# Optimization experiments

Measured on AMD Instinct MI355X. Metric: run time of the kernel, lower is better.

The kernel has to match this reference:

```python
import jax, jax.numpy as jnp
import numpy as np

S, D, H, DH = 4096, 768, 12, 64
POST_SCALE = float(np.sqrt(384.0))  # division by sqrt(1/384)


def setup_inputs() -> dict:
    key = jax.random.key(0)
    ks = jax.random.split(key, 9)
    std = 1.0 / np.sqrt(D)
    mk = lambda k: (jax.random.uniform(k, (D, D), jnp.float32, -std, std))
    return {
        "x": jax.random.normal(ks[0], (S, D), jnp.float32),
        "Wq": mk(ks[1]), "bq": jax.random.uniform(ks[2], (D,), jnp.float32, -std, std),
        "Wk": mk(ks[3]), "bk": jax.random.uniform(ks[4], (D,), jnp.float32, -std, std),
        "Wv": mk(ks[5]), "bv": jax.random.uniform(ks[6], (D,), jnp.float32, -std, std),
        "Wo": mk(ks[7]), "bo": jax.random.uniform(ks[8], (D,), jnp.float32, -std, std),
    }


def reference(x, Wq, bq, Wk, bk, Wv, bv, Wo, bo):
    # Linear layers (torch convention: y = x @ W.T + b)
    q = (x @ Wq.T + bq).reshape(S, H, DH).transpose(1, 2, 0)  # [H, DH, S]
    k = (x @ Wk.T + bk).reshape(S, H, DH).transpose(1, 0, 2)  # [H, S, DH]
    v = (x @ Wv.T + bv).reshape(S, H, DH).transpose(1, 0, 2)  # [H, S, DH]
    scores = jnp.einsum('hsd,hdt->hst', k, q)                 # [H, S, S] = k @ q
    # nn.Softmax() on a 3-D tensor legacy-defaults to dim=0 (head axis);
    # then post-softmax scale by 1/sqrt(1/384) = sqrt(384)
    attn = jax.nn.softmax(scores, axis=0) * POST_SCALE
    out = jnp.einsum('hst,htd->hsd', attn, v)                 # [H, S, DH]
    out = out.transpose(1, 0, 2).reshape(S, D)                # [S, 768]
    return out @ Wo.T + bo
```

## Files before the change

kernel.cpp:

```cpp
#include <hip/hip_runtime.h>

#define DEVINL __device__ __forceinline__

typedef __attribute__((ext_vector_type(8))) short bf16x8;
typedef __attribute__((ext_vector_type(4))) float f32x4;

static constexpr int S = 4096;
static constexpr int D = 768;
static constexpr float POST_SCALE = 19.595917942265423f;

#define MFMA16(a, b, c) __builtin_amdgcn_mfma_f32_16x16x32_bf16((a), (b), (c), 0, 0, 0)

DEVINL unsigned short f2bf(float f) {
  union { float f; unsigned u; } v; v.f = f;
  unsigned r = (v.u + 0x7FFFu + ((v.u >> 16) & 1u)) >> 16;
  return (unsigned short)r;
}

__global__ void cvt_kernel(const float* __restrict__ src,
                           unsigned short* __restrict__ dst, int n4) {
  int i = blockIdx.x * blockDim.x + threadIdx.x;
  if (i >= n4) return;
  float4 v = reinterpret_cast<const float4*>(src)[i];
  ushort4 o;
  o.x = f2bf(v.x); o.y = f2bf(v.y); o.z = f2bf(v.z); o.w = f2bf(v.w);
  reinterpret_cast<ushort4*>(dst)[i] = o;
}

__global__ void addcvt_kernel(const float* __restrict__ a,
                              const float* __restrict__ b,
                              unsigned short* __restrict__ dst, int n4) {
  int i = blockIdx.x * blockDim.x + threadIdx.x;
  if (i >= n4) return;
  float4 va = reinterpret_cast<const float4*>(a)[i];
  float4 vb = reinterpret_cast<const float4*>(b)[i];
  ushort4 o;
  o.x = f2bf(va.x + vb.x); o.y = f2bf(va.y + vb.y);
  o.z = f2bf(va.z + vb.z); o.w = f2bf(va.w + vb.w);
  reinterpret_cast<ushort4*>(dst)[i] = o;
}

__global__ void transpose_kernel(const unsigned short* __restrict__ in,
                                 unsigned short* __restrict__ out) {
  __shared__ unsigned short tile[32][33];
  int d0 = blockIdx.x * 32, t0 = blockIdx.y * 32;
  int tx = threadIdx.x, ty = threadIdx.y;
#pragma unroll
  for (int j = 0; j < 4; j++)
    tile[ty + j * 8][tx] = in[(size_t)(t0 + ty + j * 8) * D + d0 + tx];
  __syncthreads();
#pragma unroll
  for (int j = 0; j < 4; j++)
    out[(size_t)(d0 + ty + j * 8) * S + t0 + tx] = tile[tx][ty + j * 8];
}

template <bool F32OUT>
__global__ __launch_bounds__(256) void gemm_bt(
    const unsigned short* __restrict__ A, const unsigned short* __restrict__ B,
    const float* __restrict__ bias, void* __restrict__ Cout,
    int M, int N, int K) {
  int w = threadIdx.x >> 6, lane = threadIdx.x & 63;
  int r = lane & 15, b = lane >> 4;
  int rowbase = blockIdx.y * 128 + (w >> 1) * 64;
  int colbase = blockIdx.x * 128 + (w & 1) * 64;
  f32x4 acc[4][4] = {};
  for (int kk = 0; kk < K; kk += 32) {
    bf16x8 af[4], bfr[4];
#pragma unroll
    for (int m = 0; m < 4; m++)
      af[m] = *reinterpret_cast<const bf16x8*>(A + (size_t)(rowbase + m * 16 + r) * K + kk + b * 8);
#pragma unroll
    for (int n = 0; n < 4; n++)
      bfr[n] = *reinterpret_cast<const bf16x8*>(B + (size_t)(colbase + n * 16 + r) * K + kk + b * 8);
#pragma unroll
    for (int m = 0; m < 4; m++)
#pragma unroll
      for (int n = 0; n < 4; n++)
        acc[m][n] = MFMA16(af[m], bfr[n], acc[m][n]);
  }
#pragma unroll
  for (int m = 0; m < 4; m++)
#pragma unroll
    for (int n = 0; n < 4; n++)
#pragma unroll
      for (int i = 0; i < 4; i++) {
        int row = rowbase + m * 16 + b * 4 + i;
        int col = colbase + n * 16 + r;
        float v = acc[m][n][i] + bias[col];
        if (F32OUT)
          reinterpret_cast<float*>(Cout)[(size_t)row * N + col] = v;
        else
          reinterpret_cast<unsigned short*>(Cout)[(size_t)row * N + col] = f2bf(v);
      }
}

__global__ __launch_bounds__(256) void attn_kernel(
    const unsigned short* __restrict__ Qb, const unsigned short* __restrict__ Kb,
    const unsigned short* __restrict__ Vt, float* __restrict__ Opart) {
  __shared__ float Slds[12][16][32];
  __shared__ unsigned short Plds[12][16][40];

  int s0 = blockIdx.x * 16;
  int th = blockIdx.y;
  int w = threadIdx.x >> 6, lane = threadIdx.x & 63;
  int r = lane & 15, b = lane >> 4;

  bf16x8 kf[3][2];
#pragma unroll
  for (int hh = 0; hh < 3; hh++) {
    int h = w * 3 + hh;
#pragma unroll
    for (int ks = 0; ks < 2; ks++)
      kf[hh][ks] = *reinterpret_cast<const bf16x8*>(
          Kb + (size_t)(s0 + r) * D + h * 64 + ks * 32 + b * 8);
  }

  f32x4 oacc[3][4] = {};

  int tbeg = th * 2048, tend = tbeg + 2048;
  for (int t0 = tbeg; t0 < tend; t0 += 32) {
#pragma unroll
    for (int hh = 0; hh < 3; hh++) {
      int h = w * 3 + hh;
#pragma unroll
      for (int ts = 0; ts < 2; ts++) {
        f32x4 c = {};
#pragma unroll
        for (int ks = 0; ks < 2; ks++) {
          bf16x8 qf = *reinterpret_cast<const bf16x8*>(
              Qb + (size_t)(t0 + ts * 16 + r) * D + h * 64 + ks * 32 + b * 8);
          c = MFMA16(kf[hh][ks], qf, c);
        }
#pragma unroll
        for (int i = 0; i < 4; i++)
          Slds[h][b * 4 + i][ts * 16 + r] = c[i];
      }
    }
    __syncthreads();

    for (int p = threadIdx.x; p < 512; p += 256) {
      int sr = p >> 5, tc = p & 31;
      float v[12];
      float m = -1e30f;
#pragma unroll
      for (int h = 0; h < 12; h++) { v[h] = Slds[h][sr][tc]; m = fmaxf(m, v[h]); }
      float sum = 0.f;
#pragma unroll
      for (int h = 0; h < 12; h++) { v[h] = __expf(v[h] - m); sum += v[h]; }
      float sc = POST_SCALE / sum;
#pragma unroll
      for (int h = 0; h < 12; h++) Plds[h][sr][tc] = f2bf(v[h] * sc);
    }
    __syncthreads();

#pragma unroll
    for (int hh = 0; hh < 3; hh++) {
      int h = w * 3 + hh;
      bf16x8 pf = *reinterpret_cast<const bf16x8*>(&Plds[h][r][b * 8]);
#pragma unroll
      for (int ds = 0; ds < 4; ds++) {
        bf16x8 vf = *reinterpret_cast<const bf16x8*>(
            Vt + (size_t)(h * 64 + ds * 16 + r) * S + t0 + b * 8);
        oacc[hh][ds] = MFMA16(pf, vf, oacc[hh][ds]);
      }
    }
    __syncthreads();
  }

  float* Op = Opart + (size_t)th * S * D;
#pragma unroll
  for (int hh = 0; hh < 3; hh++)
#pragma unroll
    for (int ds = 0; ds < 4; ds++)
#pragma unroll
      for (int i = 0; i < 4; i++) {
        int row = s0 + b * 4 + i;
        int col = (w * 3 + hh) * 64 + ds * 16 + r;
        Op[(size_t)row * D + col] = oacc[hh][ds][i];
      }
}

extern "C" void kernel_launch(void* const* d_in, const int* in_sizes, int n_in,
                              void* d_out, int out_size, void* d_ws, size_t ws_size,
                              hipStream_t stream) {
  const float* x  = (const float*)d_in[0];
  const float* Wq = (const float*)d_in[1];
  const float* bq = (const float*)d_in[2];
  const float* Wk = (const float*)d_in[3];
  const float* bk = (const float*)d_in[4];
  const float* Wv = (const float*)d_in[5];
  const float* bv = (const float*)d_in[6];
  const float* Wo = (const float*)d_in[7];
  const float* bo = (const float*)d_in[8];
  float* out = (float*)d_out;

  char* ws = (char*)d_ws;
  size_t off = 0;
  auto walloc = [&](size_t bytes) -> void* {
    void* p = ws + off;
    off += (bytes + 255) & ~(size_t)255;
    return p;
  };
  unsigned short* xb  = (unsigned short*)walloc((size_t)S * D * 2);
  unsigned short* Wqb = (unsigned short*)walloc((size_t)D * D * 2);
  unsigned short* Wkb = (unsigned short*)walloc((size_t)D * D * 2);
  unsigned short* Wvb = (unsigned short*)walloc((size_t)D * D * 2);
  unsigned short* Wob = (unsigned short*)walloc((size_t)D * D * 2);
  unsigned short* Qb  = (unsigned short*)walloc((size_t)S * D * 2);
  unsigned short* Kb  = (unsigned short*)walloc((size_t)S * D * 2);
  unsigned short* Vb  = (unsigned short*)walloc((size_t)S * D * 2);
  unsigned short* Vt  = (unsigned short*)walloc((size_t)S * D * 2);
  unsigned short* Ob  = (unsigned short*)walloc((size_t)S * D * 2);
  float* Opart = (float*)walloc((size_t)2 * S * D * 4);

  int n4;
  n4 = S * D / 4;
  cvt_kernel<<<(n4 + 255) / 256, 256, 0, stream>>>(x, xb, n4);
  n4 = D * D / 4;
  cvt_kernel<<<(n4 + 255) / 256, 256, 0, stream>>>(Wq, Wqb, n4);
  cvt_kernel<<<(n4 + 255) / 256, 256, 0, stream>>>(Wk, Wkb, n4);
  cvt_kernel<<<(n4 + 255) / 256, 256, 0, stream>>>(Wv, Wvb, n4);
  cvt_kernel<<<(n4 + 255) / 256, 256, 0, stream>>>(Wo, Wob, n4);

  dim3 gg(D / 128, S / 128);
  gemm_bt<false><<<gg, 256, 0, stream>>>(xb, Wqb, bq, Qb, S, D, D);
  gemm_bt<false><<<gg, 256, 0, stream>>>(xb, Wkb, bk, Kb, S, D, D);
  gemm_bt<false><<<gg, 256, 0, stream>>>(xb, Wvb, bv, Vb, S, D, D);

  transpose_kernel<<<dim3(D / 32, S / 32), dim3(32, 8), 0, stream>>>(Vb, Vt);

  attn_kernel<<<dim3(S / 16, 2), 256, 0, stream>>>(Qb, Kb, Vt, Opart);

  n4 = S * D / 4;
  addcvt_kernel<<<(n4 + 255) / 256, 256, 0, stream>>>(Opart, Opart + (size_t)S * D, Ob, n4);

  gemm_bt<true><<<gg, 256, 0, stream>>>(Ob, Wob, bo, out, S, D, D);
}
```

Before: 552.0 us.

## Restructure attention kernel: register softmax across heads, 64-wide t tiles, 3-way split

The attention kernel now computes all 12 heads' scores for a 16-t slice per wave, keeping them in registers so the cross-head softmax runs without an fp32 LDS round trip. K is staged in swizzled LDS and P is written as packed bf16 via v_cvt_pk_bf16_f32. The t loop steps by 64 with two MFMAs per PV tile, and the t range is split three ways for more blocks, with launch bounds set to 3 blocks. The cost is a third partial buffer, a three-way reduction pass, and an uneven last slice.

New measurement: 553.9 us. Within noise of the previous version (+0.3%).

```diff
diff --git a/kernel.cpp b/kernel.cpp
--- a/kernel.cpp
+++ b/kernel.cpp
@@ -4,10 +4,12 @@
 
 typedef __attribute__((ext_vector_type(8))) short bf16x8;
 typedef __attribute__((ext_vector_type(4))) float f32x4;
+typedef __attribute__((ext_vector_type(2))) unsigned int u32x2;
 
 static constexpr int S = 4096;
 static constexpr int D = 768;
 static constexpr float POST_SCALE = 19.595917942265423f;
+static constexpr int TSLICE = 1344;
 
 #define MFMA16(a, b, c) __builtin_amdgcn_mfma_f32_16x16x32_bf16((a), (b), (c), 0, 0, 0)
 
@@ -27,16 +29,18 @@
   reinterpret_cast<ushort4*>(dst)[i] = o;
 }
 
-__global__ void addcvt_kernel(const float* __restrict__ a,
-                              const float* __restrict__ b,
-                              unsigned short* __restrict__ dst, int n4) {
+__global__ void addcvt3_kernel(const float* __restrict__ a,
+                               const float* __restrict__ b,
+                               const float* __restrict__ c,
+                               unsigned short* __restrict__ dst, int n4) {
   int i = blockIdx.x * blockDim.x + threadIdx.x;
   if (i >= n4) return;
   float4 va = reinterpret_cast<const float4*>(a)[i];
   float4 vb = reinterpret_cast<const float4*>(b)[i];
+  float4 vc = reinterpret_cast<const float4*>(c)[i];
   ushort4 o;
-  o.x = f2bf(va.x + vb.x); o.y = f2bf(va.y + vb.y);
-  o.z = f2bf(va.z + vb.z); o.w = f2bf(va.w + vb.w);
+  o.x = f2bf(va.x + vb.x + vc.x); o.y = f2bf(va.y + vb.y + vc.y);
+  o.z = f2bf(va.z + vb.z + vc.z); o.w = f2bf(va.w + vb.w + vc.w);
   reinterpret_cast<ushort4*>(dst)[i] = o;
 }
 
@@ -94,80 +98,103 @@
       }
 }
 
-__global__ __launch_bounds__(256) void attn_kernel(
+__global__ __launch_bounds__(256, 3) void attn_kernel(
     const unsigned short* __restrict__ Qb, const unsigned short* __restrict__ Kb,
     const unsigned short* __restrict__ Vt, float* __restrict__ Opart) {
-  __shared__ float Slds[12][16][32];
-  __shared__ unsigned short Plds[12][16][40];
-
-  int s0 = blockIdx.x * 16;
-  int th = blockIdx.y;
-  int w = threadIdx.x >> 6, lane = threadIdx.x & 63;
-  int r = lane & 15, b = lane >> 4;
-
-  bf16x8 kf[3][2];
-#pragma unroll
-  for (int hh = 0; hh < 3; hh++) {
-    int h = w * 3 + hh;
-#pragma unroll
-    for (int ks = 0; ks < 2; ks++)
-      kf[hh][ks] = *reinterpret_cast<const bf16x8*>(
-          Kb + (size_t)(s0 + r) * D + h * 64 + ks * 32 + b * 8);
+  __shared__ unsigned short K_lds[16 * 768];
+  __shared__ unsigned short P_lds[12 * 16 * 64];
+
+  const int s0 = blockIdx.x * 16;
+  const int tbeg = blockIdx.y * TSLICE;
+  const int tend = (blockIdx.y == 2) ? S : tbeg + TSLICE;
+  const int w = threadIdx.x >> 6, lane = threadIdx.x & 63;
+  const int r = lane & 15, b = lane >> 4;
+  const int swzr = (r & 7) << 4;
+
+  {
+    char* Kc = reinterpret_cast<char*>(K_lds);
+    for (int c = threadIdx.x; c < 16 * 96; c += 256) {
+      int row = c / 96, col8 = c % 96;
+      bf16x8 v = *reinterpret_cast<const bf16x8*>(Kb + (size_t)(s0 + row) * D + col8 * 8);
+      *reinterpret_cast<bf16x8*>(Kc + ((row * 1536 + col8 * 16) ^ ((row & 7) << 4))) = v;
+    }
   }
+  __syncthreads();
+
+  const char* kb0 = reinterpret_cast<const char*>(K_lds) + r * 1536 + ((b * 16) ^ swzr);
+  const char* kb1 = reinterpret_cast<const char*>(K_lds) + r * 1536 + ((64 + b * 16) ^ swzr);
+  char* pw = reinterpret_cast<char*>(P_lds) + r * 128 + ((w * 32 + b * 8) ^ swzr);
+  const char* pr0 = reinterpret_cast<const char*>(P_lds) + (w * 3) * 2048 + r * 128 + ((b * 16) ^ swzr);
+  const char* pr1 = reinterpret_cast<const char*>(P_lds) + (w * 3) * 2048 + r * 128 + ((64 + b * 16) ^ swzr);
 
   f32x4 oacc[3][4] = {};
 
-  int tbeg = th * 2048, tend = tbeg + 2048;
-  for (int t0 = tbeg; t0 < tend; t0 += 32) {
+  for (int t0 = tbeg; t0 < tend; t0 += 64) {
+    const int tw = t0 + w * 16;
+    const unsigned short* qrow = Qb + (size_t)(tw + r) * D + b * 8;
+
+    f32x4 acc[12];
+#pragma unroll
+    for (int h = 0; h < 12; h++) {
+      f32x4 c = {};
+      bf16x8 qf0 = *reinterpret_cast<const bf16x8*>(qrow + h * 64);
+      bf16x8 kf0 = *reinterpret_cast<const bf16x8*>(kb0 + h * 128);
+      c = MFMA16(qf0, kf0, c);
+      bf16x8 qf1 = *reinterpret_cast<const bf16x8*>(qrow + h * 64 + 32);
+      bf16x8 kf1 = *reinterpret_cast<const bf16x8*>(kb1 + h * 128);
+      c = MFMA16(qf1, kf1, c);
+      acc[h] = c;
+    }
+
+    float m0, m1, m2, m3, s0f, s1f, s2f, s3f;
+    m0 = acc[0][0]; m1 = acc[0][1]; m2 = acc[0][2]; m3 = acc[0][3];
+#pragma unroll
+    for (int h = 1; h < 12; h++) {
+      m0 = fmaxf(m0, acc[h][0]); m1 = fmaxf(m1, acc[h][1]);
+      m2 = fmaxf(m2, acc[h][2]); m3 = fmaxf(m3, acc[h][3]);
+    }
+    s0f = s1f = s2f = s3f = 0.f;
+#pragma unroll
+    for (int h = 0; h < 12; h++) {
+      acc[h][0] = __expf(acc[h][0] - m0); s0f += acc[h][0];
+      acc[h][1] = __expf(acc[h][1] - m1); s1f += acc[h][1];
+      acc[h][2] = __expf(acc[h][2] - m2); s2f += acc[h][2];
+      acc[h][3] = __expf(acc[h][3] - m3); s3f += acc[h][3];
+    }
+    s0f = POST_SCALE * __builtin_amdgcn_rcpf(s0f);
+    s1f = POST_SCALE * __builtin_amdgcn_rcpf(s1f);
+    s2f = POST_SCALE * __builtin_amdgcn_rcpf(s2f);
+    s3f = POST_SCALE * __builtin_amdgcn_rcpf(s3f);
+
+#pragma unroll
+    for (int h = 0; h < 12; h++) {
+      u32x2 pk;
+      float p0 = acc[h][0] * s0f, p1 = acc[h][1] * s1f;
+      float p2 = acc[h][2] * s2f, p3 = acc[h][3] * s3f;
+      asm("v_cvt_pk_bf16_f32 %0, %1, %2" : "=v"(pk.x) : "v"(p0), "v"(p1));
+      asm("v_cvt_pk_bf16_f32 %0, %1, %2" : "=v"(pk.y) : "v"(p2), "v"(p3));
+      *reinterpret_cast<u32x2*>(pw + h * 2048) = pk;
+    }
+    __syncthreads();
+
 #pragma unroll
     for (int hh = 0; hh < 3; hh++) {
-      int h = w * 3 + hh;
-#pragma unroll
-      for (int ts = 0; ts < 2; ts++) {
-        f32x4 c = {};
-#pragma unroll
-        for (int ks = 0; ks < 2; ks++) {
-          bf16x8 qf = *reinterpret_cast<const bf16x8*>(
-              Qb + (size_t)(t0 + ts * 16 + r) * D + h * 64 + ks * 32 + b * 8);
-          c = MFMA16(kf[hh][ks], qf, c);
-        }
-#pragma unroll
-        for (int i = 0; i < 4; i++)
-          Slds[h][b * 4 + i][ts * 16 + r] = c[i];
-      }
-    }
-    __syncthreads();
-
-    for (int p = threadIdx.x; p < 512; p += 256) {
-      int sr = p >> 5, tc = p & 31;
-      float v[12];
-      float m = -1e30f;
-#pragma unroll
-      for (int h = 0; h < 12; h++) { v[h] = Slds[h][sr][tc]; m = fmaxf(m, v[h]); }
-      float sum = 0.f;
-#pragma unroll
-      for (int h = 0; h < 12; h++) { v[h] = __expf(v[h] - m); sum += v[h]; }
-      float sc = POST_SCALE / sum;
-#pragma unroll
-      for (int h = 0; h < 12; h++) Plds[h][sr][tc] = f2bf(v[h] * sc);
-    }
-    __syncthreads();
-
-#pragma unroll
-    for (int hh = 0; hh < 3; hh++) {
-      int h = w * 3 + hh;
-      bf16x8 pf = *reinterpret_cast<const bf16x8*>(&Plds[h][r][b * 8]);
+      const int h = w * 3 + hh;
+      bf16x8 pf0 = *reinterpret_cast<const bf16x8*>(pr0 + hh * 2048);
+      bf16x8 pf1 = *reinterpret_cast<const bf16x8*>(pr1 + hh * 2048);
+      const unsigned short* vp = Vt + (size_t)(h * 64 + r) * S + t0 + b * 8;
 #pragma unroll
       for (int ds = 0; ds < 4; ds++) {
-        bf16x8 vf = *reinterpret_cast<const bf16x8*>(
-            Vt + (size_t)(h * 64 + ds * 16 + r) * S + t0 + b * 8);
-        oacc[hh][ds] = MFMA16(pf, vf, oacc[hh][ds]);
+        bf16x8 vf0 = *reinterpret_cast<const bf16x8*>(vp + (size_t)ds * 16 * S);
+        bf16x8 vf1 = *reinterpret_cast<const bf16x8*>(vp + (size_t)ds * 16 * S + 32);
+        oacc[hh][ds] = MFMA16(pf0, vf0, oacc[hh][ds]);
+        oacc[hh][ds] = MFMA16(pf1, vf1, oacc[hh][ds]);
       }
     }
     __syncthreads();
   }
 
-  float* Op = Opart + (size_t)th * S * D;
+  float* Op = Opart + (size_t)blockIdx.y * S * D;
 #pragma unroll
   for (int hh = 0; hh < 3; hh++)
 #pragma unroll
@@ -211,7 +238,7 @@
   unsigned short* Vb  = (unsigned short*)walloc((size_t)S * D * 2);
   unsigned short* Vt  = (unsigned short*)walloc((size_t)S * D * 2);
   unsigned short* Ob  = (unsigned short*)walloc((size_t)S * D * 2);
-  float* Opart = (float*)walloc((size_t)2 * S * D * 4);
+  float* Opart = (float*)walloc((size_t)3 * S * D * 4);
 
   int n4;
   n4 = S * D / 4;
@@ -229,10 +256,11 @@
 
   transpose_kernel<<<dim3(D / 32, S / 32), dim3(32, 8), 0, stream>>>(Vb, Vt);
 
-  attn_kernel<<<dim3(S / 16, 2), 256, 0, stream>>>(Qb, Kb, Vt, Opart);
+  attn_kernel<<<dim3(S / 16, 3), 256, 0, stream>>>(Qb, Kb, Vt, Opart);
 
   n4 = S * D / 4;
-  addcvt_kernel<<<(n4 + 255) / 256, 256, 0, stream>>>(Opart, Opart + (size_t)S * D, Ob, n4);
+  addcvt3_kernel<<<(n4 + 255) / 256, 256, 0, stream>>>(
+      Opart, Opart + (size_t)S * D, Opart + (size_t)2 * S * D, Ob, n4);
 
   gemm_bt<true><<<gg, 256, 0, stream>>>(Ob, Wob, bo, out, S, D, D);
 }
```
